# Kernel tuning notes

Measured on AMD Instinct MI355X. Metric: run time of the kernel, lower is better.

The kernel has to match this reference:

```python
import jax, jax.numpy as jnp
import numpy as np

B, C, H, W = 16, 3, 224, 224
P = 16
DIM = 256
NL = 8
DS = 16          # d_state (mamba default)
DCONV = 4
NCLS = 1000
DI = 2 * DIM     # expand * dim
DTR = -(-DIM // 16)  # dt_rank = ceil(dim/16)
NPATCH = (H // P) * (W // P)
SEQ = NPATCH + 1


def _ln(x, g, b, eps=1e-5):
    mu = x.mean(-1, keepdims=True)
    var = ((x - mu) ** 2).mean(-1, keepdims=True)
    return (x - mu) * jax.lax.rsqrt(var + eps) * g + b


def setup_inputs() -> dict:
    key = jax.random.key(0)
    ks = jax.random.split(key, 12)
    pd = C * P * P
    s = 0.02
    return dict(
        img=jax.random.normal(ks[0], (B, C, H, W), jnp.float32),
        pe_ln1_g=jnp.ones((pd,), jnp.float32), pe_ln1_b=jnp.zeros((pd,), jnp.float32),
        pe_w=jax.random.normal(ks[1], (pd, DIM), jnp.float32) * s,
        pe_b=jnp.zeros((DIM,), jnp.float32),
        pe_ln2_g=jnp.ones((DIM,), jnp.float32), pe_ln2_b=jnp.zeros((DIM,), jnp.float32),
        pos_emb=jax.random.normal(ks[2], (1, SEQ, DIM), jnp.float32) * s,
        cls_tok=jax.random.normal(ks[3], (1, 1, DIM), jnp.float32) * s,
        ln_w=jnp.ones((NL, DIM), jnp.float32), ln_b=jnp.zeros((NL, DIM), jnp.float32),
        in_w=jax.random.normal(ks[4], (NL, DIM, 2 * DI), jnp.float32) * s,
        conv_w=jax.random.normal(ks[5], (NL, DI, DCONV), jnp.float32) * s,
        conv_b=jnp.zeros((NL, DI), jnp.float32),
        xproj_w=jax.random.normal(ks[6], (NL, DI, DTR + 2 * DS), jnp.float32) * s,
        dtproj_w=jax.random.normal(ks[7], (NL, DTR, DI), jnp.float32) * s,
        dtproj_b=jax.random.uniform(ks[8], (NL, DI), jnp.float32, -4.0, -2.0),
        A_log=jnp.log(jnp.broadcast_to(jnp.arange(1, DS + 1, dtype=jnp.float32), (NL, DI, DS))) + jnp.zeros((NL, DI, DS), jnp.float32),
        Dp=jnp.ones((NL, DI), jnp.float32),
        out_w=jax.random.normal(ks[9], (NL, DI, DIM), jnp.float32) * s,
        normf_w=jnp.ones((DIM,), jnp.float32), normf_b=jnp.zeros((DIM,), jnp.float32),
        head_w=jax.random.normal(ks[10], (DIM, NCLS), jnp.float32) * s,
        head_b=jnp.zeros((NCLS,), jnp.float32),
    )


def _mamba(x, in_w, conv_w, conv_b, xproj_w, dtproj_w, dtproj_b, A_log, Dp, out_w):
    b, L, _ = x.shape
    xz = x @ in_w                       # (b, L, 2*DI)
    xm, z = jnp.split(xz, 2, axis=-1)
    # causal depthwise conv1d (torch pads both sides then slices -> left-pad d_conv-1)
    xc = jnp.pad(xm.transpose(0, 2, 1), ((0, 0), (0, 0), (DCONV - 1, 0)))
    xc = jax.lax.conv_general_dilated(
        xc, conv_w[:, None, :], (1,), 'VALID',
        dimension_numbers=('NCH', 'OIH', 'NCH'), feature_group_count=DI)
    u = jax.nn.silu(xc + conv_b[None, :, None]).transpose(0, 2, 1)  # (b, L, DI)
    dbc = u @ xproj_w                   # (b, L, DTR+2*DS)
    dt, Bm, Cm = jnp.split(dbc, [DTR, DTR + DS], axis=-1)
    dt = jax.nn.softplus(dt @ dtproj_w + dtproj_b)  # (b, L, DI)
    A = -jnp.exp(A_log)                 # (DI, DS)

    def step(h, inp):
        dt_t, B_t, C_t, u_t = inp       # (b,DI), (b,DS), (b,DS), (b,DI)
        dA = jnp.exp(dt_t[:, :, None] * A)                 # (b, DI, DS)
        h = dA * h + (dt_t * u_t)[:, :, None] * B_t[:, None, :]
        y = jnp.einsum('bdn,bn->bd', h, C_t)
        return h, y

    h0 = jnp.zeros((b, DI, DS), x.dtype)
    xs = (dt.transpose(1, 0, 2), Bm.transpose(1, 0, 2),
          Cm.transpose(1, 0, 2), u.transpose(1, 0, 2))
    _, ys = jax.lax.scan(step, h0, xs)
    y = ys.transpose(1, 0, 2) + u * Dp  # (b, L, DI)
    y = y * jax.nn.silu(z)
    return y @ out_w                    # (b, L, DIM)


def reference(img, pe_ln1_g, pe_ln1_b, pe_w, pe_b, pe_ln2_g, pe_ln2_b, pos_emb,
              cls_tok, ln_w, ln_b, in_w, conv_w, conv_b, xproj_w, dtproj_w,
              dtproj_b, A_log, Dp, out_w, normf_w, normf_b, head_w, head_b):
    b = img.shape[0]
    h, w = H // P, W // P
    # 'b c (h p1) (w p2) -> b (h w) (p1 p2 c)'
    x = img.reshape(b, C, h, P, w, P).transpose(0, 2, 4, 3, 5, 1).reshape(b, h * w, P * P * C)
    x = _ln(x, pe_ln1_g, pe_ln1_b)
    x = x @ pe_w + pe_b
    x = _ln(x, pe_ln2_g, pe_ln2_b)
    x = jnp.concatenate([jnp.broadcast_to(cls_tok, (b, 1, DIM)), x], axis=1)
    x = x + pos_emb[:, :x.shape[1]]
    residual = None
    for i in range(NL):
        residual = x if residual is None else x + residual
        xn = _ln(residual, ln_w[i], ln_b[i])
        x = _mamba(xn, in_w[i], conv_w[i], conv_b[i], xproj_w[i],
                   dtproj_w[i], dtproj_b[i], A_log[i], Dp[i], out_w[i])
    residual = x + residual
    x = _ln(residual, normf_w, normf_b)
    x = x[:, 0]                          # pool == 'cls'
    return x @ head_w + head_b
```

## Files before the change

kernel.cpp:

```cpp
#include <hip/hip_runtime.h>
#include <math.h>

#define NB   16
#define SEQL 197
#define TB   (NB*SEQL)
#define DIMM 256
#define DI   512
#define DS   16
#define NL   8

typedef __bf16 bf16x8 __attribute__((ext_vector_type(8)));
typedef __bf16 bf16x4 __attribute__((ext_vector_type(4)));
typedef float floatx4 __attribute__((ext_vector_type(4)));

__device__ __forceinline__ void block_reduce_2(float& s1, float& s2, float* red, int tid){
  #pragma unroll
  for (int off = 32; off > 0; off >>= 1){
    s1 += __shfl_down(s1, off, 64);
    s2 += __shfl_down(s2, off, 64);
  }
  __syncthreads();
  if ((tid & 63) == 0){ red[(tid>>6)*2] = s1; red[(tid>>6)*2+1] = s2; }
  __syncthreads();
  s1 = red[0] + red[2] + red[4] + red[6];
  s2 = red[1] + red[3] + red[5] + red[7];
}

__global__ __launch_bounds__(256) void transpose_bf16(
    const float* __restrict__ in, __bf16* __restrict__ out, int K, int N)
{
  __shared__ float t[32][33];
  const float* src = in  + (size_t)blockIdx.z*K*N;
  __bf16*      dst = out + (size_t)blockIdx.z*K*N;
  int n0 = blockIdx.x*32, k0 = blockIdx.y*32;
  int tx = threadIdx.x & 31, ty = threadIdx.x >> 5;
  #pragma unroll
  for (int j = 0; j < 4; j++)
    t[ty + j*8][tx] = src[(size_t)(k0 + ty + j*8)*N + n0 + tx];
  __syncthreads();
  #pragma unroll
  for (int j = 0; j < 4; j++)
    dst[(size_t)(n0 + ty + j*8)*K + k0 + tx] = (__bf16)t[tx][ty + j*8];
}

__global__ __launch_bounds__(256) void transpose_bf16_pad(
    const float* __restrict__ in, __bf16* __restrict__ out, int K, int Nin, int Npad)
{
  __shared__ float t[32][33];
  const float* src = in  + (size_t)blockIdx.z*K*Nin;
  __bf16*      dst = out + (size_t)blockIdx.z*Npad*K;
  int n0 = blockIdx.x*32, k0 = blockIdx.y*32;
  int tx = threadIdx.x & 31, ty = threadIdx.x >> 5;
  #pragma unroll
  for (int j = 0; j < 4; j++){
    int n = n0 + tx;
    t[ty + j*8][tx] = (n < Nin) ? src[(size_t)(k0 + ty + j*8)*Nin + n] : 0.f;
  }
  __syncthreads();
  #pragma unroll
  for (int j = 0; j < 4; j++)
    dst[(size_t)(n0 + ty + j*8)*K + k0 + tx] = (__bf16)t[tx][ty + j*8];
}

template<int BM, int BN>
__global__ __launch_bounds__(256) void gemm_bf16(
    const __bf16* __restrict__ A, const __bf16* __restrict__ Wt,
    const float* __restrict__ bias, float* __restrict__ C, int M, int N, int K)
{
  constexpr int BK  = 32;
  constexpr int LDA = BK + 8;
  constexpr int TMW = BM/32;
  constexpr int TNW = BN/32;
  __shared__ __bf16 As[BM][LDA];
  __shared__ __bf16 Bs[BN][LDA];

  int tid  = threadIdx.x;
  int lane = tid & 63, w = tid >> 6;
  int wm = w >> 1, wn = w & 1;
  int l15 = lane & 15, quad = lane >> 4;
  int bm = blockIdx.y * BM, bn = blockIdx.x * BN;

  floatx4 acc[TMW][TNW] = {};

  for (int k0 = 0; k0 < K; k0 += BK){
    #pragma unroll
    for (int i = 0; i < BM/64; i++){
      int c = tid + i*256;
      int row = c >> 2, kc = c & 3;
      int m = bm + row;
      uint4 v = make_uint4(0,0,0,0);
      if (m < M) v = ((const uint4*)(A + (size_t)m*K + k0))[kc];
      *(uint4*)&As[row][kc*8] = v;
    }
    #pragma unroll
    for (int i = 0; i < BN/64; i++){
      int c = tid + i*256;
      int row = c >> 2, kc = c & 3;
      int n = bn + row;
      uint4 v = ((const uint4*)(Wt + (size_t)n*K + k0))[kc];
      *(uint4*)&Bs[row][kc*8] = v;
    }
    __syncthreads();
    bf16x8 af[TMW], bf[TNW];
    #pragma unroll
    for (int mi = 0; mi < TMW; mi++)
      af[mi] = *(const bf16x8*)&As[wm*(BM/2) + mi*16 + l15][quad*8];
    #pragma unroll
    for (int ni = 0; ni < TNW; ni++)
      bf[ni] = *(const bf16x8*)&Bs[wn*(BN/2) + ni*16 + l15][quad*8];
    #pragma unroll
    for (int mi = 0; mi < TMW; mi++)
      #pragma unroll
      for (int ni = 0; ni < TNW; ni++)
        acc[mi][ni] = __builtin_amdgcn_mfma_f32_16x16x32_bf16(af[mi], bf[ni], acc[mi][ni], 0, 0, 0);
    __syncthreads();
  }
  #pragma unroll
  for (int mi = 0; mi < TMW; mi++){
    #pragma unroll
    for (int ni = 0; ni < TNW; ni++){
      int col = bn + wn*(BN/2) + ni*16 + l15;
      float bv = bias ? bias[col] : 0.f;
      #pragma unroll
      for (int r = 0; r < 4; r++){
        int row = bm + wm*(BM/2) + mi*16 + quad*4 + r;
        if (row < M) C[(size_t)row*N + col] = acc[mi][ni][r] + bv;
      }
    }
  }
}

__global__ __launch_bounds__(256) void patch_ln1(
    const float* __restrict__ img, const float* __restrict__ g1, const float* __restrict__ b1,
    __bf16* __restrict__ xp_bf)
{
  __shared__ float red[8];
  int blk = blockIdx.x;
  int b = blk / 196, p = blk % 196;
  int hh = p / 14, ww = p % 14;
  int tid = threadIdx.x;

  float v[3]; float s = 0.f, s2 = 0.f;
  #pragma unroll
  for (int i = 0; i < 3; i++){
    int e  = tid + i*256;
    int c  = e % 3;
    int p2 = (e/3) % 16;
    int p1 = e / 48;
    float val = img[((b*3 + c)*224 + hh*16 + p1)*224 + ww*16 + p2];
    v[i] = val; s += val; s2 += val*val;
  }
  block_reduce_2(s, s2, red, tid);
  float mu = s * (1.f/768.f);
  float var = s2 * (1.f/768.f) - mu*mu;
  float rr = rsqrtf(var + 1e-5f);
  #pragma unroll
  for (int i = 0; i < 3; i++){
    int e = tid + i*256;
    xp_bf[(size_t)blk*768 + e] = (__bf16)((v[i] - mu) * rr * g1[e] + b1[e]);
  }
}

__global__ __launch_bounds__(256) void ln2_cls_pos(
    const float* __restrict__ pemb, const float* __restrict__ g2, const float* __restrict__ b2,
    const float* __restrict__ pos, const float* __restrict__ cls, float* __restrict__ x)
{
  __shared__ float red[8];
  int blk = blockIdx.x;
  int b = blk / SEQL, l = blk % SEQL;
  int tid = threadIdx.x;
  if (l == 0){
    x[(size_t)b*SEQL*256 + tid] = cls[tid] + pos[tid];
    return;
  }
  int p = l - 1;
  float v = pemb[(size_t)(b*196 + p)*256 + tid];
  float s = v, s2 = v*v;
  block_reduce_2(s, s2, red, tid);
  float mu = s * (1.f/256.f);
  float var = s2 * (1.f/256.f) - mu*mu;
  float rr = rsqrtf(var + 1e-5f);
  float o = (v - mu) * rr * g2[tid] + b2[tid] + pos[(1+p)*256 + tid];
  x[((size_t)(b*SEQL + 1 + p))*256 + tid] = o;
}

__global__ __launch_bounds__(256) void add_ln(
    const float* __restrict__ x, float* __restrict__ resid, __bf16* __restrict__ xn_bf,
    const float* __restrict__ g, const float* __restrict__ bta, int first)
{
  int w = threadIdx.x >> 6, l = threadIdx.x & 63;
  int t = blockIdx.x*4 + w;
  size_t base = (size_t)t*256 + l*4;
  float4 xv = *(const float4*)&x[base];
  if (!first){
    float4 rv = *(const float4*)&resid[base];
    xv.x += rv.x; xv.y += rv.y; xv.z += rv.z; xv.w += rv.w;
  }
  *(float4*)&resid[base] = xv;
  float s  = xv.x + xv.y + xv.z + xv.w;
  float s2 = xv.x*xv.x + xv.y*xv.y + xv.z*xv.z + xv.w*xv.w;
  #pragma unroll
  for (int off = 1; off < 64; off <<= 1){
    s  += __shfl_xor(s,  off, 64);
    s2 += __shfl_xor(s2, off, 64);
  }
  float mu = s * (1.f/256.f);
  float var = s2 * (1.f/256.f) - mu*mu;
  float rr = rsqrtf(var + 1e-5f);
  float4 gv = *(const float4*)&g[l*4];
  float4 bv = *(const float4*)&bta[l*4];
  bf16x4 o;
  o[0] = (__bf16)((xv.x - mu)*rr*gv.x + bv.x);
  o[1] = (__bf16)((xv.y - mu)*rr*gv.y + bv.y);
  o[2] = (__bf16)((xv.z - mu)*rr*gv.z + bv.z);
  o[3] = (__bf16)((xv.w - mu)*rr*gv.w + bv.w);
  *(bf16x4*)&xn_bf[base] = o;
}

__global__ __launch_bounds__(256) void conv_silu(
    const float* __restrict__ xz, const float* __restrict__ cw, const float* __restrict__ cb,
    float* __restrict__ u, __bf16* __restrict__ u_bf)
{
  int gid = blockIdx.x*256 + threadIdx.x;
  int dq = gid & 127;
  int t = gid >> 7;
  int d = dq*4;
  int l = t % SEQL;
  const float4 z4 = make_float4(0.f,0.f,0.f,0.f);
  float4 x0 = *(const float4*)&xz[(size_t)t*1024 + d];
  float4 x1 = (l>=1) ? *(const float4*)&xz[(size_t)(t-1)*1024 + d] : z4;
  float4 x2 = (l>=2) ? *(const float4*)&xz[(size_t)(t-2)*1024 + d] : z4;
  float4 x3 = (l>=3) ? *(const float4*)&xz[(size_t)(t-3)*1024 + d] : z4;
  float4 w0 = *(const float4*)&cw[(d+0)*4];
  float4 w1 = *(const float4*)&cw[(d+1)*4];
  float4 w2 = *(const float4*)&cw[(d+2)*4];
  float4 w3 = *(const float4*)&cw[(d+3)*4];
  float4 r = *(const float4*)&cb[d];
  r.x += x3.x*w0.x + x2.x*w0.y + x1.x*w0.z + x0.x*w0.w;
  r.y += x3.y*w1.x + x2.y*w1.y + x1.y*w1.z + x0.y*w1.w;
  r.z += x3.z*w2.x + x2.z*w2.y + x1.z*w2.z + x0.z*w2.w;
  r.w += x3.w*w3.x + x2.w*w3.y + x1.w*w3.z + x0.w*w3.w;
  r.x *= 1.f/(1.f + __expf(-r.x));
  r.y *= 1.f/(1.f + __expf(-r.y));
  r.z *= 1.f/(1.f + __expf(-r.z));
  r.w *= 1.f/(1.f + __expf(-r.w));
  *(float4*)&u[(size_t)t*512 + d] = r;
  bf16x4 o; o[0]=(__bf16)r.x; o[1]=(__bf16)r.y; o[2]=(__bf16)r.z; o[3]=(__bf16)r.w;
  *(bf16x4*)&u_bf[(size_t)t*512 + d] = o;
}

#define SCT 32
#define NCH ((SEQL + SCT - 1)/SCT)
#define NDL 8
__global__ __launch_bounds__(128) void scan_kernel(
    const float* __restrict__ u, const float* __restrict__ dbc,
    const float* __restrict__ xz, const float* __restrict__ A_log, const float* __restrict__ Dp,
    const float* __restrict__ dtw, const float* __restrict__ dtb,
    __bf16* __restrict__ yg_bf)
{
  __shared__ float s_D [16][36];
  __shared__ float s_B [16][36];
  __shared__ float s_C [16][36];
  __shared__ float s_u [NDL][36];
  __shared__ float s_z [NDL][36];
  __shared__ float s_dt[NDL][36];
  __shared__ float s_yp[SCT][NDL][20];
  __shared__ float s_dp[NDL];

  int tid = threadIdx.x;
  int n = tid & 15, dl = tid >> 4;
  int b = blockIdx.x >> 6, dg = blockIdx.x & 63;
  int d0 = dg * NDL;
  const size_t base = (size_t)b * SEQL;

  float A = -__expf(A_log[(d0+dl)*DS + n]);
  float h = 0.f;
  if (tid < NDL) s_dp[tid] = Dp[d0 + tid];
  int cch = tid & 7;
  float wc[16];
  #pragma unroll
  for (int k = 0; k < 16; k++) wc[k] = dtw[k*512 + d0 + cch];
  float dtbv = dtb[d0 + cch];

  float r_u[2], r_z[2], r_db[12];
  auto load_regs = [&](int c){
    #pragma unroll
    for (int i = 0; i < 2; i++){
      int v = tid + i*128;
      int tg = c*SCT + (v>>3); if (tg > SEQL-1) tg = SEQL-1;
      size_t t = base + tg;
      r_u[i] = u [t*512 + d0 + (v&7)];
      r_z[i] = xz[t*1024 + 512 + d0 + (v&7)];
    }
    #pragma unroll
    for (int s = 0; s < 3; s++)
      #pragma unroll
      for (int i = 0; i < 4; i++){
        int v = tid + i*128;
        int tg = c*SCT + (v>>4); if (tg > SEQL-1) tg = SEQL-1;
        r_db[s*4+i] = dbc[(base + tg)*64 + s*16 + (v&15)];
      }
  };
  auto write_DBC = [&](){
    #pragma unroll
    for (int i = 0; i < 4; i++){
      int v = tid + i*128;
      s_D[v&15][v>>4] = r_db[0+i];
      s_B[v&15][v>>4] = r_db[4+i];
      s_C[v&15][v>>4] = r_db[8+i];
    }
  };
  auto write_UZ = [&](){
    #pragma unroll
    for (int i = 0; i < 2; i++){
      int v = tid + i*128;
      s_u[v&7][v>>3] = r_u[i];
      s_z[v&7][v>>3] = r_z[i];
    }
  };
  auto compute_dt = [&](){
    #pragma unroll
    for (int i = 0; i < 2; i++){
      int tl = (tid >> 3) + i*16;
      float acc = dtbv;
      #pragma unroll
      for (int k = 0; k < 16; k++) acc += s_D[k][tl] * wc[k];
      s_dt[cch][tl] = (acc > 20.f) ? acc : log1pf(__expf(acc));
    }
  };

  load_regs(0);
  write_DBC();
  write_UZ();
  __syncthreads();
  compute_dt();
  __syncthreads();

  for (int c = 0; c < NCH; c++){
    if (c + 1 < NCH) load_regs(c+1);

    float4 dt4, u4, B4, C4;
    #pragma unroll
    for (int tl = 0; tl < SCT; tl++){
      if ((tl & 3) == 0){
        dt4 = *(const float4*)&s_dt[dl][tl];
        u4  = *(const float4*)&s_u [dl][tl];
        B4  = *(const float4*)&s_B [n][tl];
        C4  = *(const float4*)&s_C [n][tl];
      }
      float dtv = ((float*)&dt4)[tl&3];
      float uv  = ((float*)&u4 )[tl&3];
      float Bv  = ((float*)&B4 )[tl&3];
      float Cv  = ((float*)&C4 )[tl&3];
      h = __expf(dtv * A) * h + (dtv * uv) * Bv;
      s_yp[tl][dl][n] = h * Cv;
    }
    __syncthreads();

    if (c + 1 < NCH) write_DBC();

    #pragma unroll
    for (int j = 0; j < 2; j++){
      int p = tid + j*128;
      int tl = p >> 3, dr = p & 7;
      float4 a0 = *(const float4*)&s_yp[tl][dr][0];
      float4 a1 = *(const float4*)&s_yp[tl][dr][4];
      float4 a2 = *(const float4*)&s_yp[tl][dr][8];
      float4 a3 = *(const float4*)&s_yp[tl][dr][12];
      float yv = ((a0.x+a0.y)+(a0.z+a0.w)) + ((a1.x+a1.y)+(a1.z+a1.w))
               + ((a2.x+a2.y)+(a2.z+a2.w)) + ((a3.x+a3.y)+(a3.z+a3.w));
      int tg = c*SCT + tl;
      if (tg < SEQL){
        float uv = s_u[dr][tl];
        float zv = s_z[dr][tl];
        float sg = 1.f / (1.f + __expf(-zv));
        yg_bf[(base + tg)*512 + d0 + dr] = (__bf16)((yv + uv*s_dp[dr]) * zv * sg);
      }
    }
    __syncthreads();

    if (c + 1 < NCH){
      write_UZ();
      compute_dt();
      __syncthreads();
    }
  }
}

__global__ __launch_bounds__(256) void final_ln(
    const float* __restrict__ x, const float* __restrict__ resid,
    const float* __restrict__ g, const float* __restrict__ bta, float* __restrict__ xs_g)
{
  __shared__ float red[8];
  int b = blockIdx.x, tid = threadIdx.x;
  size_t idx = (size_t)b*SEQL*256 + tid;
  float r = x[idx] + resid[idx];
  float s = r, s2 = r*r;
  block_reduce_2(s, s2, red, tid);
  float mu = s * (1.f/256.f);
  float var = s2 * (1.f/256.f) - mu*mu;
  float rr = rsqrtf(var + 1e-5f);
  xs_g[b*256 + tid] = (r - mu) * rr * g[tid] + bta[tid];
}

__global__ __launch_bounds__(256) void head_gemm(
    const float* __restrict__ xs_g, const float* __restrict__ head_w,
    const float* __restrict__ head_b, float* __restrict__ out)
{
  __shared__ float xs[16][256];
  int tid = threadIdx.x;
  #pragma unroll
  for (int i = 0; i < 16; i++) ((float*)xs)[tid + i*256] = xs_g[tid + i*256];
  __syncthreads();
  int nl = tid & 31, bq = tid >> 5;
  int nn = blockIdx.x*32 + nl;
  if (nn >= 1000) return;
  float acc0 = 0.f, acc1 = 0.f;
  #pragma unroll 8
  for (int k = 0; k < 256; k++){
    float w = head_w[k*1000 + nn];
    acc0 += xs[bq][k]   * w;
    acc1 += xs[bq+8][k] * w;
  }
  float hb = head_b[nn];
  out[(size_t)bq*1000 + nn]     = acc0 + hb;
  out[(size_t)(bq+8)*1000 + nn] = acc1 + hb;
}

extern "C" void kernel_launch(void* const* d_in, const int* in_sizes, int n_in,
                              void* d_out, int out_size, void* d_ws, size_t ws_size,
                              hipStream_t stream) {
  const float* img   = (const float*)d_in[0];
  const float* ln1g  = (const float*)d_in[1];
  const float* ln1b  = (const float*)d_in[2];
  const float* pe_w  = (const float*)d_in[3];
  const float* pe_b  = (const float*)d_in[4];
  const float* ln2g  = (const float*)d_in[5];
  const float* ln2b  = (const float*)d_in[6];
  const float* pos   = (const float*)d_in[7];
  const float* cls   = (const float*)d_in[8];
  const float* ln_w  = (const float*)d_in[9];
  const float* ln_b  = (const float*)d_in[10];
  const float* in_w  = (const float*)d_in[11];
  const float* conv_w= (const float*)d_in[12];
  const float* conv_b= (const float*)d_in[13];
  const float* xproj = (const float*)d_in[14];
  const float* dtw   = (const float*)d_in[15];
  const float* dtb   = (const float*)d_in[16];
  const float* A_log = (const float*)d_in[17];
  const float* Dp    = (const float*)d_in[18];
  const float* out_w = (const float*)d_in[19];
  const float* nfw   = (const float*)d_in[20];
  const float* nfb   = (const float*)d_in[21];
  const float* head_w= (const float*)d_in[22];
  const float* head_b= (const float*)d_in[23];
  float* out = (float*)d_out;

  float* ws = (float*)d_ws;
  float* x     = ws;  ws += (size_t)TB*DIMM;
  float* resid = ws;  ws += (size_t)TB*DIMM;
  float* xz    = ws;  ws += (size_t)TB*2*DI;
  float* u     = ws;  ws += (size_t)TB*DI;
  float* dbc   = ws;  ws += (size_t)TB*64;
  float* xs_g  = ws;  ws += (size_t)NB*DIMM;
  __bf16* xn_bf = (__bf16*)ws;  ws += (size_t)TB*DIMM/2;
  __bf16* u_bf  = (__bf16*)ws;  ws += (size_t)TB*DI/2;
  __bf16* yg_bf = (__bf16*)ws;  ws += (size_t)TB*DI/2;
  __bf16* wt_in = (__bf16*)ws;  ws += (size_t)NL*1024*256/2;
  __bf16* wt_out= (__bf16*)ws;  ws += (size_t)NL*256*512/2;
  __bf16* wt_pe = (__bf16*)ws;  ws += (size_t)256*768/2;
  __bf16* wt_xp = (__bf16*)ws;  ws += (size_t)NL*64*512/2;
  __bf16* xp_bf = (__bf16*)xz;
  float*  pemb  = u;

  transpose_bf16<<<dim3(1024/32, 256/32, NL), 256, 0, stream>>>(in_w,  wt_in, 256, 1024);
  transpose_bf16<<<dim3( 256/32, 512/32, NL), 256, 0, stream>>>(out_w, wt_out, 512, 256);
  transpose_bf16<<<dim3( 256/32, 768/32,  1), 256, 0, stream>>>(pe_w,  wt_pe, 768, 256);
  transpose_bf16_pad<<<dim3(2, 512/32, NL), 256, 0, stream>>>(xproj, wt_xp, 512, 48, 64);

  patch_ln1<<<NB*196, 256, 0, stream>>>(img, ln1g, ln1b, xp_bf);
  gemm_bf16<64,64><<<dim3(256/64, 3136/64), 256, 0, stream>>>(
      xp_bf, wt_pe, pe_b, pemb, 3136, 256, 768);
  ln2_cls_pos<<<NB*SEQL, 256, 0, stream>>>(pemb, ln2g, ln2b, pos, cls, x);

  for (int i = 0; i < NL; i++){
    add_ln<<<TB/4, 256, 0, stream>>>(x, resid, xn_bf, ln_w + i*DIMM, ln_b + i*DIMM, i == 0 ? 1 : 0);
    gemm_bf16<64,128><<<dim3(1024/128, (TB+63)/64), 256, 0, stream>>>(
        xn_bf, wt_in + (size_t)i*1024*256, nullptr, xz, TB, 1024, 256);
    conv_silu<<<TB*128/256, 256, 0, stream>>>(
        xz, conv_w + i*DI*4, conv_b + i*DI, u, u_bf);
    gemm_bf16<64,64><<<dim3(1, (TB+63)/64), 256, 0, stream>>>(
        u_bf, wt_xp + (size_t)i*64*512, nullptr, dbc, TB, 64, 512);
    scan_kernel<<<NB*64, 128, 0, stream>>>(
        u, dbc, xz, A_log + i*DI*DS, Dp + i*DI, dtw + i*16*DI, dtb + i*DI, yg_bf);
    gemm_bf16<64,64><<<dim3(4, (TB+63)/64), 256, 0, stream>>>(
        yg_bf, wt_out + (size_t)i*256*512, nullptr, x, TB, DIMM, 512);
  }
  final_ln<<<NB, 256, 0, stream>>>(x, resid, nfw, nfb, xs_g);
  head_gemm<<<(1000+31)/32, 256, 0, stream>>>(xs_g, head_w, head_b, out);
}
```

Measured before the change: 719.0 us.

## Split selective scan into chunked parallel passes with carry propagation

```diff
diff --git a/kernel.cpp b/kernel.cpp
--- a/kernel.cpp
+++ b/kernel.cpp
@@ -8,6 +8,11 @@
 #define DI   512
 #define DS   16
 #define NL   8
+
+#define SCT 32
+#define NCH ((SEQL + SCT - 1)/SCT)
+#define NDL 8
+#define NCHAIN (NB*DI*DS)
 
 typedef __bf16 bf16x8 __attribute__((ext_vector_type(8)));
 typedef __bf16 bf16x4 __attribute__((ext_vector_type(4)));
@@ -249,14 +254,100 @@
   *(bf16x4*)&u_bf[(size_t)t*512 + d] = o;
 }
 
-#define SCT 32
-#define NCH ((SEQL + SCT - 1)/SCT)
-#define NDL 8
-__global__ __launch_bounds__(128) void scan_kernel(
+
+__global__ __launch_bounds__(128) void scan_part(
+    const float* __restrict__ u, const float* __restrict__ dbc,
+    const float* __restrict__ A_log,
+    const float* __restrict__ dtw, const float* __restrict__ dtb,
+    float* __restrict__ hL_g, float* __restrict__ P_g)
+{
+  __shared__ float s_D [16][36];
+  __shared__ float s_B [16][36];
+  __shared__ float s_u [NDL][36];
+  __shared__ float s_dt[NDL][36];
+
+  int tid = threadIdx.x;
+  int n = tid & 15, dl = tid >> 4;
+  int bid = blockIdx.x;
+  int c  = bid / (NB*64);
+  int rem = bid - c*(NB*64);
+  int b = rem >> 6, dg = rem & 63;
+  int d0 = dg * NDL;
+  const size_t base = (size_t)b * SEQL;
+
+  float A = -__expf(A_log[(d0+dl)*DS + n]);
+  int cch = tid & 7;
+  float wc[16];
+  #pragma unroll
+  for (int k = 0; k < 16; k++) wc[k] = dtw[k*512 + d0 + cch];
+  float dtbv = dtb[d0 + cch];
+
+  #pragma unroll
+  for (int i = 0; i < 2; i++){
+    int v = tid + i*128;
+    int tg = c*SCT + (v>>3); if (tg > SEQL-1) tg = SEQL-1;
+    s_u[v&7][v>>3] = u[(base + tg)*512 + d0 + (v&7)];
+  }
+  #pragma unroll
+  for (int s = 0; s < 2; s++)
+    #pragma unroll
+    for (int i = 0; i < 4; i++){
+      int v = tid + i*128;
+      int tg = c*SCT + (v>>4); if (tg > SEQL-1) tg = SEQL-1;
+      float val = dbc[(base + tg)*64 + s*16 + (v&15)];
+      if (s == 0) s_D[v&15][v>>4] = val; else s_B[v&15][v>>4] = val;
+    }
+  __syncthreads();
+  #pragma unroll
+  for (int i = 0; i < 2; i++){
+    int tl = (tid >> 3) + i*16;
+    float acc = dtbv;
+    #pragma unroll
+    for (int k = 0; k < 16; k++) acc += s_D[k][tl] * wc[k];
+    s_dt[cch][tl] = (acc > 20.f) ? acc : log1pf(__expf(acc));
+  }
+  __syncthreads();
+
+  float h = 0.f, P = 1.f;
+  float4 dt4, u4, B4;
+  #pragma unroll
+  for (int tl = 0; tl < SCT; tl++){
+    if ((tl & 3) == 0){
+      dt4 = *(const float4*)&s_dt[dl][tl];
+      u4  = *(const float4*)&s_u [dl][tl];
+      B4  = *(const float4*)&s_B [n][tl];
+    }
+    float dtv = ((float*)&dt4)[tl&3];
+    float uv  = ((float*)&u4 )[tl&3];
+    float Bv  = ((float*)&B4 )[tl&3];
+    float a = __expf(dtv * A);
+    h = a * h + (dtv * uv) * Bv;
+    P *= a;
+  }
+  int chain = b*8192 + d0*16 + tid;
+  hL_g[(size_t)c*NCHAIN + chain] = h;
+  P_g [(size_t)c*NCHAIN + chain] = P;
+}
+
+__global__ __launch_bounds__(256) void scan_carry(
+    const float* __restrict__ hL_g, const float* __restrict__ P_g,
+    float* __restrict__ Hc_g)
+{
+  int chain = blockIdx.x*256 + threadIdx.x;
+  float H = 0.f;
+  #pragma unroll
+  for (int c = 0; c < NCH; c++){
+    Hc_g[(size_t)c*NCHAIN + chain] = H;
+    if (c < NCH-1)
+      H = hL_g[(size_t)c*NCHAIN + chain] + P_g[(size_t)c*NCHAIN + chain] * H;
+  }
+}
+
+__global__ __launch_bounds__(128) void scan_final(
     const float* __restrict__ u, const float* __restrict__ dbc,
     const float* __restrict__ xz, const float* __restrict__ A_log, const float* __restrict__ Dp,
     const float* __restrict__ dtw, const float* __restrict__ dtb,
-    __bf16* __restrict__ yg_bf)
+    const float* __restrict__ Hc_g, __bf16* __restrict__ yg_bf)
 {
   __shared__ float s_D [16][36];
   __shared__ float s_B [16][36];
@@ -269,120 +360,90 @@
 
   int tid = threadIdx.x;
   int n = tid & 15, dl = tid >> 4;
-  int b = blockIdx.x >> 6, dg = blockIdx.x & 63;
+  int bid = blockIdx.x;
+  int c  = bid / (NB*64);
+  int rem = bid - c*(NB*64);
+  int b = rem >> 6, dg = rem & 63;
   int d0 = dg * NDL;
   const size_t base = (size_t)b * SEQL;
 
   float A = -__expf(A_log[(d0+dl)*DS + n]);
-  float h = 0.f;
   if (tid < NDL) s_dp[tid] = Dp[d0 + tid];
   int cch = tid & 7;
   float wc[16];
   #pragma unroll
   for (int k = 0; k < 16; k++) wc[k] = dtw[k*512 + d0 + cch];
   float dtbv = dtb[d0 + cch];
-
-  float r_u[2], r_z[2], r_db[12];
-  auto load_regs = [&](int c){
-    #pragma unroll
-    for (int i = 0; i < 2; i++){
-      int v = tid + i*128;
-      int tg = c*SCT + (v>>3); if (tg > SEQL-1) tg = SEQL-1;
-      size_t t = base + tg;
-      r_u[i] = u [t*512 + d0 + (v&7)];
-      r_z[i] = xz[t*1024 + 512 + d0 + (v&7)];
-    }
-    #pragma unroll
-    for (int s = 0; s < 3; s++)
-      #pragma unroll
-      for (int i = 0; i < 4; i++){
-        int v = tid + i*128;
-        int tg = c*SCT + (v>>4); if (tg > SEQL-1) tg = SEQL-1;
-        r_db[s*4+i] = dbc[(base + tg)*64 + s*16 + (v&15)];
-      }
-  };
-  auto write_DBC = [&](){
+  int chain = b*8192 + d0*16 + tid;
+  float H = Hc_g[(size_t)c*NCHAIN + chain];
+
+  #pragma unroll
+  for (int i = 0; i < 2; i++){
+    int v = tid + i*128;
+    int tg = c*SCT + (v>>3); if (tg > SEQL-1) tg = SEQL-1;
+    size_t t = base + tg;
+    s_u[v&7][v>>3] = u [t*512 + d0 + (v&7)];
+    s_z[v&7][v>>3] = xz[t*1024 + 512 + d0 + (v&7)];
+  }
+  #pragma unroll
+  for (int s = 0; s < 3; s++)
     #pragma unroll
     for (int i = 0; i < 4; i++){
       int v = tid + i*128;
-      s_D[v&15][v>>4] = r_db[0+i];
-      s_B[v&15][v>>4] = r_db[4+i];
-      s_C[v&15][v>>4] = r_db[8+i];
-    }
-  };
-  auto write_UZ = [&](){
-    #pragma unroll
-    for (int i = 0; i < 2; i++){
-      int v = tid + i*128;
-      s_u[v&7][v>>3] = r_u[i];
-      s_z[v&7][v>>3] = r_z[i];
-    }
-  };
-  auto compute_dt = [&](){
-    #pragma unroll
-    for (int i = 0; i < 2; i++){
-      int tl = (tid >> 3) + i*16;
-      float acc = dtbv;
-      #pragma unroll
-      for (int k = 0; k < 16; k++) acc += s_D[k][tl] * wc[k];
-      s_dt[cch][tl] = (acc > 20.f) ? acc : log1pf(__expf(acc));
-    }
-  };
-
-  load_regs(0);
-  write_DBC();
-  write_UZ();
-  __syncthreads();
-  compute_dt();
-  __syncthreads();
-
-  for (int c = 0; c < NCH; c++){
-    if (c + 1 < NCH) load_regs(c+1);
-
-    float4 dt4, u4, B4, C4;
-    #pragma unroll
-    for (int tl = 0; tl < SCT; tl++){
-      if ((tl & 3) == 0){
-        dt4 = *(const float4*)&s_dt[dl][tl];
-        u4  = *(const float4*)&s_u [dl][tl];
-        B4  = *(const float4*)&s_B [n][tl];
-        C4  = *(const float4*)&s_C [n][tl];
-      }
-      float dtv = ((float*)&dt4)[tl&3];
-      float uv  = ((float*)&u4 )[tl&3];
-      float Bv  = ((float*)&B4 )[tl&3];
-      float Cv  = ((float*)&C4 )[tl&3];
-      h = __expf(dtv * A) * h + (dtv * uv) * Bv;
-      s_yp[tl][dl][n] = h * Cv;
-    }
-    __syncthreads();
-
-    if (c + 1 < NCH) write_DBC();
-
-    #pragma unroll
-    for (int j = 0; j < 2; j++){
-      int p = tid + j*128;
-      int tl = p >> 3, dr = p & 7;
-      float4 a0 = *(const float4*)&s_yp[tl][dr][0];
-      float4 a1 = *(const float4*)&s_yp[tl][dr][4];
-      float4 a2 = *(const float4*)&s_yp[tl][dr][8];
-      float4 a3 = *(const float4*)&s_yp[tl][dr][12];
-      float yv = ((a0.x+a0.y)+(a0.z+a0.w)) + ((a1.x+a1.y)+(a1.z+a1.w))
-               + ((a2.x+a2.y)+(a2.z+a2.w)) + ((a3.x+a3.y)+(a3.z+a3.w));
-      int tg = c*SCT + tl;
-      if (tg < SEQL){
-        float uv = s_u[dr][tl];
-        float zv = s_z[dr][tl];
-        float sg = 1.f / (1.f + __expf(-zv));
-        yg_bf[(base + tg)*512 + d0 + dr] = (__bf16)((yv + uv*s_dp[dr]) * zv * sg);
-      }
-    }
-    __syncthreads();
-
-    if (c + 1 < NCH){
-      write_UZ();
-      compute_dt();
-      __syncthreads();
+      int tg = c*SCT + (v>>4); if (tg > SEQL-1) tg = SEQL-1;
+      float val = dbc[(base + tg)*64 + s*16 + (v&15)];
+      if (s == 0)      s_D[v&15][v>>4] = val;
+      else if (s == 1) s_B[v&15][v>>4] = val;
+      else             s_C[v&15][v>>4] = val;
+    }
+  __syncthreads();
+  #pragma unroll
+  for (int i = 0; i < 2; i++){
+    int tl = (tid >> 3) + i*16;
+    float acc = dtbv;
+    #pragma unroll
+    for (int k = 0; k < 16; k++) acc += s_D[k][tl] * wc[k];
+    s_dt[cch][tl] = (acc > 20.f) ? acc : log1pf(__expf(acc));
+  }
+  __syncthreads();
+
+  float h = 0.f, P = 1.f;
+  float4 dt4, u4, B4, C4;
+  #pragma unroll
+  for (int tl = 0; tl < SCT; tl++){
+    if ((tl & 3) == 0){
+      dt4 = *(const float4*)&s_dt[dl][tl];
+      u4  = *(const float4*)&s_u [dl][tl];
+      B4  = *(const float4*)&s_B [n][tl];
+      C4  = *(const float4*)&s_C [n][tl];
+    }
+    float dtv = ((float*)&dt4)[tl&3];
+    float uv  = ((float*)&u4 )[tl&3];
+    float Bv  = ((float*)&B4 )[tl&3];
+    float Cv  = ((float*)&C4 )[tl&3];
+    float a = __expf(dtv * A);
+    h = a * h + (dtv * uv) * Bv;
+    P *= a;
+    s_yp[tl][dl][n] = (h + P*H) * Cv;
+  }
+  __syncthreads();
+
+  #pragma unroll
+  for (int j = 0; j < 2; j++){
+    int p = tid + j*128;
+    int tl = p >> 3, dr = p & 7;
+    float4 a0 = *(const float4*)&s_yp[tl][dr][0];
+    float4 a1 = *(const float4*)&s_yp[tl][dr][4];
+    float4 a2 = *(const float4*)&s_yp[tl][dr][8];
+    float4 a3 = *(const float4*)&s_yp[tl][dr][12];
+    float yv = ((a0.x+a0.y)+(a0.z+a0.w)) + ((a1.x+a1.y)+(a1.z+a1.w))
+             + ((a2.x+a2.y)+(a2.z+a2.w)) + ((a3.x+a3.y)+(a3.z+a3.w));
+    int tg = c*SCT + tl;
+    if (tg < SEQL){
+      float uv = s_u[dr][tl];
+      float zv = s_z[dr][tl];
+      float sg = 1.f / (1.f + __expf(-zv));
+      yg_bf[(base + tg)*512 + d0 + dr] = (__bf16)((yv + uv*s_dp[dr]) * zv * sg);
     }
   }
 }
@@ -463,6 +524,9 @@
   float* u     = ws;  ws += (size_t)TB*DI;
   float* dbc   = ws;  ws += (size_t)TB*64;
   float* xs_g  = ws;  ws += (size_t)NB*DIMM;
+  float* hL_g  = ws;  ws += (size_t)(NCH-1)*NCHAIN;
+  float* P_g   = ws;  ws += (size_t)(NCH-1)*NCHAIN;
+  float* Hc_g  = ws;  ws += (size_t)NCH*NCHAIN;
   __bf16* xn_bf = (__bf16*)ws;  ws += (size_t)TB*DIMM/2;
   __bf16* u_bf  = (__bf16*)ws;  ws += (size_t)TB*DI/2;
   __bf16* yg_bf = (__bf16*)ws;  ws += (size_t)TB*DI/2;
@@ -485,14 +549,17 @@
 
   for (int i = 0; i < NL; i++){
     add_ln<<<TB/4, 256, 0, stream>>>(x, resid, xn_bf, ln_w + i*DIMM, ln_b + i*DIMM, i == 0 ? 1 : 0);
-    gemm_bf16<64,128><<<dim3(1024/128, (TB+63)/64), 256, 0, stream>>>(
+    gemm_bf16<128,128><<<dim3(1024/128, (TB+127)/128), 256, 0, stream>>>(
         xn_bf, wt_in + (size_t)i*1024*256, nullptr, xz, TB, 1024, 256);
     conv_silu<<<TB*128/256, 256, 0, stream>>>(
         xz, conv_w + i*DI*4, conv_b + i*DI, u, u_bf);
     gemm_bf16<64,64><<<dim3(1, (TB+63)/64), 256, 0, stream>>>(
         u_bf, wt_xp + (size_t)i*64*512, nullptr, dbc, TB, 64, 512);
-    scan_kernel<<<NB*64, 128, 0, stream>>>(
-        u, dbc, xz, A_log + i*DI*DS, Dp + i*DI, dtw + i*16*DI, dtb + i*DI, yg_bf);
+    scan_part<<<(NCH-1)*NB*64, 128, 0, stream>>>(
+        u, dbc, A_log + i*DI*DS, dtw + i*16*DI, dtb + i*DI, hL_g, P_g);
+    scan_carry<<<NCHAIN/256, 256, 0, stream>>>(hL_g, P_g, Hc_g);
+    scan_final<<<NCH*NB*64, 128, 0, stream>>>(
+        u, dbc, xz, A_log + i*DI*DS, Dp + i*DI, dtw + i*16*DI, dtb + i*DI, Hc_g, yg_bf);
     gemm_bf16<64,64><<<dim3(4, (TB+63)/64), 256, 0, stream>>>(
         yg_bf, wt_out + (size_t)i*256*512, nullptr, x, TB, DIMM, 512);
   }
```

After: 924.8 us. +28.6%, slower.
